# Kernel tuning notes

Hardware: AMD Instinct MI355X
Metric: run time of the kernel (lower is better)

Reference implementation:

```python
import jax, jax.numpy as jnp
import numpy as np

TMP = 1.0          # concrete temperature (beta)
SAMPLE_BIAS = 0.0  # self.sample_bias

N_NODES = 10000
N_EDGES = 640000
D_EMB = 128
HIDDEN = 64


def setup_inputs() -> dict:
    key = jax.random.key(0)
    k_emb, k_ei, k_w1, k_w2 = jax.random.split(key, 4)
    embed = jax.random.normal(k_emb, (N_NODES, D_EMB), dtype=jnp.float32)
    edge_index = jax.random.randint(k_ei, (2, N_EDGES), 0, N_NODES, dtype=jnp.int64)
    W1 = jax.random.normal(k_w1, (2 * D_EMB, HIDDEN), dtype=jnp.float32) * 0.06
    b1 = jnp.zeros((HIDDEN,), dtype=jnp.float32)
    W2 = jax.random.normal(k_w2, (HIDDEN, 1), dtype=jnp.float32) * 0.12
    b2 = jnp.zeros((1,), dtype=jnp.float32)
    return {"embed": embed, "edge_index": edge_index, "W1": W1, "b1": b1, "W2": W2, "b2": b2}


def _concrete_sample(log_alpha, beta, key):
    # training=True branch: logistic noise through sigmoid gate
    u = jax.random.uniform(key, log_alpha.shape, dtype=log_alpha.dtype)
    u = u * (1.0 - 2.0 * SAMPLE_BIAS) + SAMPLE_BIAS
    noise = jnp.log(u) - jnp.log1p(-u)
    return jax.nn.sigmoid((noise + log_alpha) / beta)


def reference(embed, edge_index, W1, b1, W2, b2):
    N = embed.shape[0]
    col, row = edge_index[0], edge_index[1]
    # edge gather + concat: [E, 2*D]
    f12 = jnp.concatenate([embed[col], embed[row]], axis=-1)
    # tiny 2-layer MLP -> per-edge logit
    h = jax.nn.relu(f12 @ W1 + b1)
    log_alpha = (h @ W2 + b2).reshape(-1)  # [E]
    values = _concrete_sample(log_alpha, TMP, jax.random.key(42))
    # sparse_coo_tensor(...).to_dense() sums duplicate indices
    adj = jnp.zeros((N, N), dtype=embed.dtype).at[col, row].add(1.0)
    mask_dense = jnp.zeros((N, N), dtype=embed.dtype).at[col, row].add(values)
    sym_mask = (mask_dense + mask_dense.T) * 0.5
    masked_adj = adj * sym_mask
    return masked_adj
```

## Files before the change

kernel.cpp:

```cpp
#include <hip/hip_runtime.h>
#include <stdint.h>

#define D_EMB 128
#define HIDDEN 64
#define PACK_SCALE 1024.0f
#define INV_PACK (1.0f/1024.0f)

__device__ __forceinline__ uint32_t rotl32(uint32_t x, int r) {
    return (x << r) | (x >> (32 - r));
}

__device__ __forceinline__ uint32_t jax_threefry_bits_part(uint32_t e) {
    const uint32_t ks0 = 0u;
    const uint32_t ks1 = 42u;
    const uint32_t ks2 = 0x1BD11BDAu ^ 0u ^ 42u;
    uint32_t x0 = 0u + ks0;
    uint32_t x1 = e + ks1;
#define TF_R(r) { x0 += x1; x1 = rotl32(x1, (r)); x1 ^= x0; }
    TF_R(13) TF_R(15) TF_R(26) TF_R(6)
    x0 += ks1; x1 += ks2 + 1u;
    TF_R(17) TF_R(29) TF_R(16) TF_R(24)
    x0 += ks2; x1 += ks0 + 2u;
    TF_R(13) TF_R(15) TF_R(26) TF_R(6)
    x0 += ks0; x1 += ks1 + 3u;
    TF_R(17) TF_R(29) TF_R(16) TF_R(24)
    x0 += ks1; x1 += ks2 + 4u;
    TF_R(13) TF_R(15) TF_R(26) TF_R(6)
    x0 += ks2; x1 += ks0 + 5u;
#undef TF_R
    return x0 ^ x1;
}

__global__ __launch_bounds__(128) void node_proj_kernel(
    const float* __restrict__ embed, const float* __restrict__ W1,
    const float* __restrict__ b1, float* __restrict__ Pcat) {
    __shared__ float e_lds[D_EMB];
    int n = blockIdx.x;
    int t = threadIdx.x;
    e_lds[t] = embed[(size_t)n * D_EMB + t];
    __syncthreads();
    int half = t >> 6;
    int k = t & 63;
    const float* w = W1 + (size_t)half * D_EMB * HIDDEN + k;
    float acc = (half == 0) ? b1[k] : 0.0f;
#pragma unroll 16
    for (int d = 0; d < D_EMB; d++) {
        acc += e_lds[d] * w[(size_t)d * HIDDEN];
    }
    Pcat[(size_t)n * (2 * HIDDEN) + t] = acc;
}

__global__ __launch_bounds__(256) void edge_scatter_kernel(
    const int* __restrict__ ei, const float* __restrict__ Pcat,
    const float* __restrict__ W2, const float* __restrict__ b2,
    float* __restrict__ out, int E, int N) {
    __shared__ float w2s[HIDDEN];
    if (threadIdx.x < HIDDEN) w2s[threadIdx.x] = W2[threadIdx.x];
    __syncthreads();
    int e = blockIdx.x * blockDim.x + threadIdx.x;
    if (e >= E) return;
    int c = ei[e];
    int r = ei[E + e];
    if ((unsigned)c >= (unsigned)N || (unsigned)r >= (unsigned)N) return;

    const float4* p1 = (const float4*)(Pcat + (size_t)c * (2 * HIDDEN));
    const float4* p2 = (const float4*)(Pcat + (size_t)r * (2 * HIDDEN) + HIDDEN);
    const float4* w4 = (const float4*)w2s;
    float la = b2[0];
#pragma unroll
    for (int k = 0; k < HIDDEN / 4; k++) {
        float4 a = p1[k];
        float4 b = p2[k];
        float4 w = w4[k];
        la += fmaxf(a.x + b.x, 0.0f) * w.x + fmaxf(a.y + b.y, 0.0f) * w.y +
              fmaxf(a.z + b.z, 0.0f) * w.z + fmaxf(a.w + b.w, 0.0f) * w.w;
    }

    uint32_t bits = jax_threefry_bits_part((uint32_t)e);
    float u = __uint_as_float((bits >> 9) | 0x3f800000u) - 1.0f;
    float v = u / (u + (1.0f - u) * __expf(-la));

    atomicAdd(out + (size_t)c * N + r, PACK_SCALE + v);
}

__global__ __launch_bounds__(256) void edge_read_kernel(
    const int* __restrict__ ei, const float* __restrict__ out,
    float* __restrict__ vals, int E, int N) {
    int e = blockIdx.x * blockDim.x + threadIdx.x;
    if (e >= E) return;
    int c = ei[e];
    int r = ei[E + e];
    if ((unsigned)c >= (unsigned)N || (unsigned)r >= (unsigned)N) { return; }
    float a = out[(size_t)c * N + r];
    float b = out[(size_t)r * N + c];
    float cnt_a = truncf(a * INV_PACK);
    float s_a = a - PACK_SCALE * cnt_a;
    float cnt_b = truncf(b * INV_PACK);
    float s_b = b - PACK_SCALE * cnt_b;
    vals[e] = cnt_a * 0.5f * (s_a + s_b);
}

__global__ __launch_bounds__(256) void edge_write_kernel(
    const int* __restrict__ ei, const float* __restrict__ vals,
    float* __restrict__ out, int E, int N) {
    int e = blockIdx.x * blockDim.x + threadIdx.x;
    if (e >= E) return;
    int c = ei[e];
    int r = ei[E + e];
    if ((unsigned)c >= (unsigned)N || (unsigned)r >= (unsigned)N) return;
    out[(size_t)c * N + r] = vals[e];
}

extern "C" void kernel_launch(void* const* d_in, const int* in_sizes, int n_in,
                              void* d_out, int out_size, void* d_ws, size_t ws_size,
                              hipStream_t stream) {
    const float* embed = (const float*)d_in[0];
    const int*   ei    = (const int*)d_in[1];
    const float* W1    = (const float*)d_in[2];
    const float* b1    = (const float*)d_in[3];
    const float* W2    = (const float*)d_in[4];
    const float* b2    = (const float*)d_in[5];
    float* out = (float*)d_out;

    const int N = in_sizes[0] / D_EMB;
    const int E = in_sizes[1] / 2;

    float* Pcat = (float*)d_ws;
    float* vals = (float*)((char*)d_ws + (size_t)N * 2 * HIDDEN * sizeof(float));

    hipMemsetAsync(d_out, 0, (size_t)out_size * sizeof(float), stream);

    node_proj_kernel<<<N, 128, 0, stream>>>(embed, W1, b1, Pcat);

    const int eb = 256;
    const int eg = (E + eb - 1) / eb;
    edge_scatter_kernel<<<eg, eb, 0, stream>>>(ei, Pcat, W2, b2, out, E, N);
    edge_read_kernel<<<eg, eb, 0, stream>>>(ei, out, vals, E, N);
    edge_write_kernel<<<eg, eb, 0, stream>>>(ei, vals, out, E, N);
}
```

Baseline: 211.3 us.

## Accumulate edge values in a compact open-addressing hash table before dense write

```diff
diff --git a/kernel.cpp b/kernel.cpp
--- a/kernel.cpp
+++ b/kernel.cpp
@@ -31,6 +31,26 @@
     return x0 ^ x1;
 }
 
+__device__ __forceinline__ float edge_gate_value(
+    const float* __restrict__ Pcat, const float* __restrict__ w2s, float b2v,
+    int c, int r, int e) {
+    const float4* p1 = (const float4*)(Pcat + (size_t)c * (2 * HIDDEN));
+    const float4* p2 = (const float4*)(Pcat + (size_t)r * (2 * HIDDEN) + HIDDEN);
+    const float4* w4 = (const float4*)w2s;
+    float la = b2v;
+#pragma unroll
+    for (int k = 0; k < HIDDEN / 4; k++) {
+        float4 a = p1[k];
+        float4 b = p2[k];
+        float4 w = w4[k];
+        la += fmaxf(a.x + b.x, 0.0f) * w.x + fmaxf(a.y + b.y, 0.0f) * w.y +
+              fmaxf(a.z + b.z, 0.0f) * w.z + fmaxf(a.w + b.w, 0.0f) * w.w;
+    }
+    uint32_t bits = jax_threefry_bits_part((uint32_t)e);
+    float u = __uint_as_float((bits >> 9) | 0x3f800000u) - 1.0f;
+    return u / (u + (1.0f - u) * __expf(-la));
+}
+
 __global__ __launch_bounds__(128) void node_proj_kernel(
     const float* __restrict__ embed, const float* __restrict__ W1,
     const float* __restrict__ b1, float* __restrict__ Pcat) {
@@ -50,6 +70,65 @@
     Pcat[(size_t)n * (2 * HIDDEN) + t] = acc;
 }
 
+
+__global__ __launch_bounds__(256) void scatter_hash_kernel(
+    const int* __restrict__ ei, const float* __restrict__ Pcat,
+    const float* __restrict__ W2, const float* __restrict__ b2,
+    uint32_t* __restrict__ tab, int E, int N, int log_sz) {
+    __shared__ float w2s[HIDDEN];
+    if (threadIdx.x < HIDDEN) w2s[threadIdx.x] = W2[threadIdx.x];
+    __syncthreads();
+    int e = blockIdx.x * blockDim.x + threadIdx.x;
+    if (e >= E) return;
+    int c = ei[e];
+    int r = ei[E + e];
+    if ((unsigned)c >= (unsigned)N || (unsigned)r >= (unsigned)N) return;
+
+    float v = edge_gate_value(Pcat, w2s, b2[0], c, r, e);
+
+    uint32_t key = (uint32_t)c * (uint32_t)N + (uint32_t)r;
+    uint32_t mask = (1u << log_sz) - 1u;
+    uint32_t h = (key * 2654435761u) >> (32 - log_sz);
+    for (;;) {
+        uint32_t prev = atomicCAS(&tab[2 * h], 0u, key + 1u);
+        if (prev == 0u || prev == key + 1u) break;
+        h = (h + 1u) & mask;
+    }
+    atomicAdd((float*)&tab[2 * h + 1], PACK_SCALE + v);
+}
+
+__device__ __forceinline__ float hash_lookup(
+    const uint32_t* __restrict__ tab, uint32_t key, int log_sz) {
+    uint32_t mask = (1u << log_sz) - 1u;
+    uint32_t h = (key * 2654435761u) >> (32 - log_sz);
+    for (;;) {
+        uint2 ent = ((const uint2*)tab)[h];
+        if (ent.x == key + 1u) return __uint_as_float(ent.y);
+        if (ent.x == 0u) return 0.0f;
+        h = (h + 1u) & mask;
+    }
+}
+
+__global__ __launch_bounds__(256) void finalize_hash_kernel(
+    const int* __restrict__ ei, const uint32_t* __restrict__ tab,
+    float* __restrict__ out, int E, int N, int log_sz) {
+    int e = blockIdx.x * blockDim.x + threadIdx.x;
+    if (e >= E) return;
+    int c = ei[e];
+    int r = ei[E + e];
+    if ((unsigned)c >= (unsigned)N || (unsigned)r >= (unsigned)N) return;
+    uint32_t kf = (uint32_t)c * (uint32_t)N + (uint32_t)r;
+    uint32_t kb = (uint32_t)r * (uint32_t)N + (uint32_t)c;
+    float a = hash_lookup(tab, kf, log_sz);
+    float b = hash_lookup(tab, kb, log_sz);
+    float cnt_a = truncf(a * INV_PACK);
+    float s_a = a - PACK_SCALE * cnt_a;
+    float cnt_b = truncf(b * INV_PACK);
+    float s_b = b - PACK_SCALE * cnt_b;
+    out[(size_t)c * N + r] = cnt_a * 0.5f * (s_a + s_b);
+}
+
+
 __global__ __launch_bounds__(256) void edge_scatter_kernel(
     const int* __restrict__ ei, const float* __restrict__ Pcat,
     const float* __restrict__ W2, const float* __restrict__ b2,
@@ -62,24 +141,7 @@
     int c = ei[e];
     int r = ei[E + e];
     if ((unsigned)c >= (unsigned)N || (unsigned)r >= (unsigned)N) return;
-
-    const float4* p1 = (const float4*)(Pcat + (size_t)c * (2 * HIDDEN));
-    const float4* p2 = (const float4*)(Pcat + (size_t)r * (2 * HIDDEN) + HIDDEN);
-    const float4* w4 = (const float4*)w2s;
-    float la = b2[0];
-#pragma unroll
-    for (int k = 0; k < HIDDEN / 4; k++) {
-        float4 a = p1[k];
-        float4 b = p2[k];
-        float4 w = w4[k];
-        la += fmaxf(a.x + b.x, 0.0f) * w.x + fmaxf(a.y + b.y, 0.0f) * w.y +
-              fmaxf(a.z + b.z, 0.0f) * w.z + fmaxf(a.w + b.w, 0.0f) * w.w;
-    }
-
-    uint32_t bits = jax_threefry_bits_part((uint32_t)e);
-    float u = __uint_as_float((bits >> 9) | 0x3f800000u) - 1.0f;
-    float v = u / (u + (1.0f - u) * __expf(-la));
-
+    float v = edge_gate_value(Pcat, w2s, b2[0], c, r, e);
     atomicAdd(out + (size_t)c * N + r, PACK_SCALE + v);
 }
 
@@ -90,7 +152,7 @@
     if (e >= E) return;
     int c = ei[e];
     int r = ei[E + e];
-    if ((unsigned)c >= (unsigned)N || (unsigned)r >= (unsigned)N) { return; }
+    if ((unsigned)c >= (unsigned)N || (unsigned)r >= (unsigned)N) return;
     float a = out[(size_t)c * N + r];
     float b = out[(size_t)r * N + c];
     float cnt_a = truncf(a * INV_PACK);
@@ -126,7 +188,13 @@
     const int E = in_sizes[1] / 2;
 
     float* Pcat = (float*)d_ws;
-    float* vals = (float*)((char*)d_ws + (size_t)N * 2 * HIDDEN * sizeof(float));
+    size_t pcat_bytes = ((size_t)N * 2 * HIDDEN * sizeof(float) + 255) & ~(size_t)255;
+    size_t avail = (ws_size > pcat_bytes) ? (ws_size - pcat_bytes) : 0;
+
+    int log_sz = 0;
+    for (int L = 22; L >= 20; L--) {
+        if (((size_t)8 << L) <= avail) { log_sz = L; break; }
+    }
 
     hipMemsetAsync(d_out, 0, (size_t)out_size * sizeof(float), stream);
 
@@ -134,7 +202,16 @@
 
     const int eb = 256;
     const int eg = (E + eb - 1) / eb;
-    edge_scatter_kernel<<<eg, eb, 0, stream>>>(ei, Pcat, W2, b2, out, E, N);
-    edge_read_kernel<<<eg, eb, 0, stream>>>(ei, out, vals, E, N);
-    edge_write_kernel<<<eg, eb, 0, stream>>>(ei, vals, out, E, N);
-}
+
+    if (log_sz >= 20) {
+        uint32_t* tab = (uint32_t*)((char*)d_ws + pcat_bytes);
+        hipMemsetAsync(tab, 0, (size_t)8 << log_sz, stream);
+        scatter_hash_kernel<<<eg, eb, 0, stream>>>(ei, Pcat, W2, b2, tab, E, N, log_sz);
+        finalize_hash_kernel<<<eg, eb, 0, stream>>>(ei, tab, out, E, N, log_sz);
+    } else {
+        float* vals = (float*)((char*)d_ws + pcat_bytes);
+        edge_scatter_kernel<<<eg, eb, 0, stream>>>(ei, Pcat, W2, b2, out, E, N);
+        edge_read_kernel<<<eg, eb, 0, stream>>>(ei, out, vals, E, N);
+        edge_write_kernel<<<eg, eb, 0, stream>>>(ei, vals, out, E, N);
+    }
+}
```

Result: slower. 239.6 us (+13.4%).

## Fuse edge read/write passes and batch node projection across nodes

Applied to the files above, without the earlier changes.

```diff
diff --git a/kernel.cpp b/kernel.cpp
--- a/kernel.cpp
+++ b/kernel.cpp
@@ -5,6 +5,7 @@
 #define HIDDEN 64
 #define PACK_SCALE 1024.0f
 #define INV_PACK (1.0f/1024.0f)
+#define NODES_PER_BLK 8
 
 __device__ __forceinline__ uint32_t rotl32(uint32_t x, int r) {
     return (x << r) | (x >> (32 - r));
@@ -31,23 +32,52 @@
     return x0 ^ x1;
 }
 
-__global__ __launch_bounds__(128) void node_proj_kernel(
+__device__ __forceinline__ float edge_gate_value(
+    const float* __restrict__ Pcat, const float* __restrict__ w2s, float b2v,
+    int c, int r, int e) {
+    const float4* p1 = (const float4*)(Pcat + (size_t)c * (2 * HIDDEN));
+    const float4* p2 = (const float4*)(Pcat + (size_t)r * (2 * HIDDEN) + HIDDEN);
+    const float4* w4 = (const float4*)w2s;
+    float la = b2v;
+#pragma unroll
+    for (int k = 0; k < HIDDEN / 4; k++) {
+        float4 a = p1[k];
+        float4 b = p2[k];
+        float4 w = w4[k];
+        la += fmaxf(a.x + b.x, 0.0f) * w.x + fmaxf(a.y + b.y, 0.0f) * w.y +
+              fmaxf(a.z + b.z, 0.0f) * w.z + fmaxf(a.w + b.w, 0.0f) * w.w;
+    }
+    uint32_t bits = jax_threefry_bits_part((uint32_t)e);
+    float u = __uint_as_float((bits >> 9) | 0x3f800000u) - 1.0f;
+    return u / (u + (1.0f - u) * __expf(-la));
+}
+
+__global__ __launch_bounds__(256) void node_proj_kernel(
     const float* __restrict__ embed, const float* __restrict__ W1,
-    const float* __restrict__ b1, float* __restrict__ Pcat) {
-    __shared__ float e_lds[D_EMB];
-    int n = blockIdx.x;
+    const float* __restrict__ b1, float* __restrict__ Pcat, int N) {
+    __shared__ float e_lds[NODES_PER_BLK][D_EMB];
+    int n0 = blockIdx.x * NODES_PER_BLK;
     int t = threadIdx.x;
-    e_lds[t] = embed[(size_t)n * D_EMB + t];
+    {
+        int node = n0 + (t >> 5);
+        float4 v = make_float4(0.f, 0.f, 0.f, 0.f);
+        if (node < N) v = ((const float4*)embed)[(size_t)n0 * (D_EMB / 4) + t];
+        ((float4*)&e_lds[0][0])[t] = v;
+    }
     __syncthreads();
-    int half = t >> 6;
-    int k = t & 63;
-    const float* w = W1 + (size_t)half * D_EMB * HIDDEN + k;
-    float acc = (half == 0) ? b1[k] : 0.0f;
+#pragma unroll
+    for (int rep = 0; rep < 4; rep++) {
+        int idx = rep * 256 + t;
+        int nl = idx >> 7;
+        int col = idx & 127;
+        int half = col >> 6, k = col & 63;
+        const float* w = W1 + (size_t)half * D_EMB * HIDDEN + k;
+        float acc = (half == 0) ? b1[k] : 0.0f;
+        const float* ev = e_lds[nl];
 #pragma unroll 16
-    for (int d = 0; d < D_EMB; d++) {
-        acc += e_lds[d] * w[(size_t)d * HIDDEN];
+        for (int d = 0; d < D_EMB; d++) acc += ev[d] * w[(size_t)d * HIDDEN];
+        if (n0 + nl < N) Pcat[(size_t)(n0 + nl) * (2 * HIDDEN) + col] = acc;
     }
-    Pcat[(size_t)n * (2 * HIDDEN) + t] = acc;
 }
 
 __global__ __launch_bounds__(256) void edge_scatter_kernel(
@@ -62,53 +92,34 @@
     int c = ei[e];
     int r = ei[E + e];
     if ((unsigned)c >= (unsigned)N || (unsigned)r >= (unsigned)N) return;
-
-    const float4* p1 = (const float4*)(Pcat + (size_t)c * (2 * HIDDEN));
-    const float4* p2 = (const float4*)(Pcat + (size_t)r * (2 * HIDDEN) + HIDDEN);
-    const float4* w4 = (const float4*)w2s;
-    float la = b2[0];
-#pragma unroll
-    for (int k = 0; k < HIDDEN / 4; k++) {
-        float4 a = p1[k];
-        float4 b = p2[k];
-        float4 w = w4[k];
-        la += fmaxf(a.x + b.x, 0.0f) * w.x + fmaxf(a.y + b.y, 0.0f) * w.y +
-              fmaxf(a.z + b.z, 0.0f) * w.z + fmaxf(a.w + b.w, 0.0f) * w.w;
-    }
-
-    uint32_t bits = jax_threefry_bits_part((uint32_t)e);
-    float u = __uint_as_float((bits >> 9) | 0x3f800000u) - 1.0f;
-    float v = u / (u + (1.0f - u) * __expf(-la));
-
+    float v = edge_gate_value(Pcat, w2s, b2[0], c, r, e);
     atomicAdd(out + (size_t)c * N + r, PACK_SCALE + v);
 }
 
-__global__ __launch_bounds__(256) void edge_read_kernel(
-    const int* __restrict__ ei, const float* __restrict__ out,
-    float* __restrict__ vals, int E, int N) {
-    int e = blockIdx.x * blockDim.x + threadIdx.x;
-    if (e >= E) return;
-    int c = ei[e];
-    int r = ei[E + e];
-    if ((unsigned)c >= (unsigned)N || (unsigned)r >= (unsigned)N) { return; }
-    float a = out[(size_t)c * N + r];
-    float b = out[(size_t)r * N + c];
-    float cnt_a = truncf(a * INV_PACK);
-    float s_a = a - PACK_SCALE * cnt_a;
-    float cnt_b = truncf(b * INV_PACK);
-    float s_b = b - PACK_SCALE * cnt_b;
-    vals[e] = cnt_a * 0.5f * (s_a + s_b);
-}
-
-__global__ __launch_bounds__(256) void edge_write_kernel(
-    const int* __restrict__ ei, const float* __restrict__ vals,
-    float* __restrict__ out, int E, int N) {
+__global__ __launch_bounds__(256) void edge_finalize_kernel(
+    const int* __restrict__ ei, float* __restrict__ out, int E, int N) {
     int e = blockIdx.x * blockDim.x + threadIdx.x;
     if (e >= E) return;
     int c = ei[e];
     int r = ei[E + e];
     if ((unsigned)c >= (unsigned)N || (unsigned)r >= (unsigned)N) return;
-    out[(size_t)c * N + r] = vals[e];
+
+    size_t own = (size_t)c * N + r;
+    size_t mir = (size_t)r * N + c;
+    float a = out[own];
+    if (a < PACK_SCALE) return;
+    float b = out[mir];
+    if (c != r && b > 0.0f && b < PACK_SCALE) return;
+
+    if (c <= r || b == 0.0f) {
+        float cnt_a = truncf(a * INV_PACK);
+        float s_a = a - PACK_SCALE * cnt_a;
+        float cnt_b = truncf(b * INV_PACK);
+        float s_b = b - PACK_SCALE * cnt_b;
+        float sum = s_a + s_b;
+        out[own] = cnt_a * 0.5f * sum;
+        if (c < r && b != 0.0f) out[mir] = cnt_b * 0.5f * sum;
+    }
 }
 
 extern "C" void kernel_launch(void* const* d_in, const int* in_sizes, int n_in,
@@ -126,15 +137,14 @@
     const int E = in_sizes[1] / 2;
 
     float* Pcat = (float*)d_ws;
-    float* vals = (float*)((char*)d_ws + (size_t)N * 2 * HIDDEN * sizeof(float));
 
     hipMemsetAsync(d_out, 0, (size_t)out_size * sizeof(float), stream);
 
-    node_proj_kernel<<<N, 128, 0, stream>>>(embed, W1, b1, Pcat);
+    node_proj_kernel<<<(N + NODES_PER_BLK - 1) / NODES_PER_BLK, 256, 0, stream>>>(
+        embed, W1, b1, Pcat, N);
 
     const int eb = 256;
     const int eg = (E + eb - 1) / eb;
     edge_scatter_kernel<<<eg, eb, 0, stream>>>(ei, Pcat, W2, b2, out, E, N);
-    edge_read_kernel<<<eg, eb, 0, stream>>>(ei, out, vals, E, N);
-    edge_write_kernel<<<eg, eb, 0, stream>>>(ei, vals, out, E, N);
+    edge_finalize_kernel<<<eg, eb, 0, stream>>>(ei, out, E, N);
 }
```

Measured after the change: 219.5 us. +3.9%, slower.
